# Kernel optimization log

Measured on AMD Instinct MI355X. Metric: run time of the kernel, lower is better.

The kernel has to match this reference:

```python
import jax, jax.numpy as jnp
import numpy as np

NUM_HEADS = 8


def setup_inputs() -> dict:
    key = jax.random.key(0)
    ks = jax.random.split(key, 6)
    B, S, H = 2, 4096, 512
    Q = jax.random.normal(ks[0], (B, S, H), dtype=jnp.float32)
    K = jax.random.normal(ks[1], (B, S, H), dtype=jnp.float32)
    V = jax.random.normal(ks[2], (B, S, H), dtype=jnp.float32)
    risk_sigma = jax.random.uniform(ks[3], (B, 1), dtype=jnp.float32) * 0.2
    risk_lambda = jnp.array([2.0], dtype=jnp.float32)
    W_out = jax.random.normal(ks[4], (H, H), dtype=jnp.float32) * (1.0 / np.sqrt(H))
    b_out = jnp.zeros((H,), dtype=jnp.float32)
    return {"Q": Q, "K": K, "V": V, "risk_sigma": risk_sigma,
            "risk_lambda": risk_lambda, "W_out": W_out, "b_out": b_out}


def reference(Q, K, V, risk_sigma, risk_lambda, W_out, b_out):
    B, S, H = Q.shape
    nh = NUM_HEADS
    hd = H // nh
    # split heads: [B, S, nh, hd]
    q = Q.reshape(B, S, nh, hd)
    k = K.reshape(B, S, nh, hd)
    v = V.reshape(B, S, nh, hd)
    scale = 1.0 / jnp.sqrt(jnp.asarray(hd, dtype=Q.dtype))
    # [B, nh, S, S]
    scores = jnp.einsum('bshd,bthd->bhst', q, k) * scale
    # distance-based risk penalty
    pos = jnp.arange(S, dtype=Q.dtype)
    norm_dist = jnp.abs(pos[None, :] - pos[:, None]) / S  # [S, S]
    dist_sq = norm_dist ** 2
    sigma_c = jnp.clip(risk_sigma, 0.001, 0.2)            # [B, 1]
    sigma_n = (sigma_c - 0.001) / (0.2 - 0.001)
    lam = (risk_lambda / 10.0).reshape(())                 # scalar
    risk_term = lam * sigma_n[:, :, None, None] * dist_sq[None, None]  # [B,1,S,S]
    attn = jax.nn.softmax(scores - risk_term, axis=-1)
    ctx = jnp.einsum('bhst,bthd->bshd', attn, v).reshape(B, S, H)
    return ctx @ W_out.T + b_out
```

## Files before the change

kernel.cpp:

```cpp
#include <hip/hip_runtime.h>
#include <hip/hip_bf16.h>


#define S_LEN 4096
#define NHEAD 8
#define HD 64
#define HTOT 512

typedef __attribute__((ext_vector_type(8))) short short8;
typedef __attribute__((ext_vector_type(4))) float floatx4;
typedef __attribute__((ext_vector_type(8))) _Float16 half8;
typedef __attribute__((ext_vector_type(2))) _Float16 half2v;

#if __has_builtin(__builtin_amdgcn_exp2f)
#define EXP2F(x) __builtin_amdgcn_exp2f(x)
#else
#define EXP2F(x) exp2f(x)
#endif

__device__ __forceinline__ unsigned pack_bf16(float a, float b) {
    unsigned ua = __builtin_bit_cast(unsigned, a) + 0x8000u;
    unsigned ub = __builtin_bit_cast(unsigned, b) + 0x8000u;
    return __builtin_amdgcn_perm(ub, ua, 0x07060302u);
}

__device__ __forceinline__ unsigned short f2bf(float x) {
    unsigned u = __builtin_bit_cast(unsigned, x) + 0x8000u;
    return (unsigned short)(u >> 16);
}

__device__ __forceinline__ void async16(const unsigned short* g, unsigned short* l) {
    __builtin_amdgcn_global_load_lds(
        (const __attribute__((address_space(1))) unsigned int*)g,
        (__attribute__((address_space(3))) unsigned int*)l, 16, 0, 0);
}

__global__ __launch_bounds__(256) void prep_kernel(
    const float* __restrict__ K, unsigned short* __restrict__ K16,
    const float* __restrict__ V, unsigned short* __restrict__ Vt,
    const float* __restrict__ W, unsigned short* __restrict__ W16)
{
    const int tid = threadIdx.x;
    if (blockIdx.x >= 3072) {
        size_t i = ((size_t)(blockIdx.x - 3072) * 256 + tid) * 8;
        float4 a = *(const float4*)(W + i);
        float4 b = *(const float4*)(W + i + 4);
        unsigned o[4] = {pack_bf16(a.x, a.y), pack_bf16(a.z, a.w),
                         pack_bf16(b.x, b.y), pack_bf16(b.z, b.w)};
        *(short8*)(W16 + i) = *(short8*)o;
    } else if (blockIdx.x < 2048) {
        size_t i = ((size_t)blockIdx.x * 256 + tid) * 8;
        float4 a = *(const float4*)(K + i);
        float4 b = *(const float4*)(K + i + 4);
        unsigned o[4] = {pack_bf16(a.x, a.y), pack_bf16(a.z, a.w),
                         pack_bf16(b.x, b.y), pack_bf16(b.z, b.w)};
        *(short8*)(K16 + i) = *(short8*)o;
    } else {
        __shared__ unsigned short T[64 * 66];
        const int blk = blockIdx.x - 2048;
        const int st = blk & 63;
        const int bh = blk >> 6;
        const int b = bh >> 3, h = bh & 7;
        const float* src = V + ((size_t)b * S_LEN + st * 64) * HTOT + h * HD;
        for (int i = 0; i < 4; i++) {
            int idx = tid + i * 256;
            int s = idx >> 4, c4 = idx & 15;
            float4 v = *(const float4*)(src + (size_t)s * HTOT + c4 * 4);
            T[(c4 * 4 + 0) * 66 + s] = f2bf(v.x);
            T[(c4 * 4 + 1) * 66 + s] = f2bf(v.y);
            T[(c4 * 4 + 2) * 66 + s] = f2bf(v.z);
            T[(c4 * 4 + 3) * 66 + s] = f2bf(v.w);
        }
        __syncthreads();
        unsigned short* dst = Vt + ((size_t)bh * 64) * S_LEN + st * 64;
        for (int i = 0; i < 2; i++) {
            int idx = tid + i * 256;
            int d = idx >> 3, c8 = idx & 7;
            uint2 lo = *(const uint2*)&T[d * 66 + c8 * 8];
            uint2 hi = *(const uint2*)&T[d * 66 + c8 * 8 + 4];
            unsigned o[4] = {lo.x, lo.y, hi.x, hi.y};
            *(short8*)(dst + (size_t)d * S_LEN + c8 * 8) = *(short8*)o;
        }
    }
}

__global__ __launch_bounds__(256) void attn_kernel(
    const float* __restrict__ Q, const unsigned short* __restrict__ K16,
    const unsigned short* __restrict__ Vt,
    const float* __restrict__ risk_sigma, const float* __restrict__ risk_lambda,
    _Float16* __restrict__ Cpart, float* __restrict__ Lpart)
{
    __shared__ unsigned short QPsh[128 * 72];
    __shared__ unsigned short Ksh[2][64 * 64];
    __shared__ unsigned short Vsh[2][64 * 64];

    const int tid  = threadIdx.x;
    const int wave = tid >> 6;
    const int lane = tid & 63;
    const int quad = lane >> 4;
    const int ln   = lane & 15;
    const int sw   = ln & 7;

    const int bid = blockIdx.x;
    const int ks  = bid & 1;
    const int qt  = (bid >> 1) & 31;
    const int h   = (bid >> 6) & 7;
    const int b   = bid >> 9;
    const int qbase = qt * 128;

    float sig = risk_sigma[b];
    sig = fminf(fmaxf(sig, 0.001f), 0.2f);
    const float sn   = (sig - 0.001f) * (1.0f / 0.199f);
    const float coef = risk_lambda[0] * 0.1f * sn;
    const float nc2 = -coef * (1.0f / 4096.0f) * (1.0f / 4096.0f) * 1.4426950408889634f;
    const float qscale = 0.125f * 1.4426950408889634f;

    const float* Qb = Q + (size_t)b * S_LEN * HTOT + (size_t)h * HD;
    const unsigned short* Kb = K16 + (size_t)b * S_LEN * HTOT + (size_t)h * HD;
    const unsigned short* Vb = Vt + ((size_t)(b * 8 + h) * 64) * S_LEN;

    const int rl  = lane >> 3;
    const int c8g = ((lane & 7) ^ rl) << 3;
    auto dma = [&](int buf, int kbase) {
        const unsigned short* gk = Kb + (size_t)(kbase + wave * 8 + rl) * HTOT + c8g;
        const unsigned short* gv = Vb + (size_t)(wave * 8 + rl) * S_LEN + kbase + c8g;
        async16(gk,              &Ksh[buf][wave * 512 + lane * 8]);
        async16(gk + 32 * HTOT,  &Ksh[buf][(wave + 4) * 512 + lane * 8]);
        async16(gv,              &Vsh[buf][wave * 512 + lane * 8]);
        async16(gv + 32 * S_LEN, &Vsh[buf][(wave + 4) * 512 + lane * 8]);
    };

    dma(0, ks * 2048);
    for (int i = 0; i < 8; i++) {
        int idx = tid + i * 256;
        int r = idx >> 4, c4 = idx & 15;
        float4 v = *(const float4*)(Qb + (size_t)(qbase + r) * HTOT + c4 * 4);
        uint2 o;
        o.x = pack_bf16(v.x * qscale, v.y * qscale);
        o.y = pack_bf16(v.z * qscale, v.w * qscale);
        *(uint2*)&QPsh[r * 72 + c4 * 4] = o;
    }
    __syncthreads();

    short8 qf[2][2];
    for (int nt = 0; nt < 2; nt++) {
        qf[nt][0] = *(const short8*)&QPsh[(wave * 32 + nt * 16 + ln) * 72 + quad * 8];
        qf[nt][1] = *(const short8*)&QPsh[(wave * 32 + nt * 16 + ln) * 72 + 32 + quad * 8];
    }
    unsigned short* Pw = &QPsh[wave * 32 * 72];

    const short sone = (short)0x3F80;
    const short8 ones = {sone, sone, sone, sone, sone, sone, sone, sone};

    floatx4 Oacc[2][4], Lacc[2];
    for (int nt = 0; nt < 2; nt++) {
        Lacc[nt] = (floatx4){0.f, 0.f, 0.f, 0.f};
        for (int dt = 0; dt < 4; dt++) Oacc[nt][dt] = (floatx4){0.f, 0.f, 0.f, 0.f};
    }

    const int qa = qbase + wave * 32;

    for (int kt = 0; kt < 32; ++kt) {
        const int kbase = ks * 2048 + kt * 64;
        const int cur = kt & 1;
        if (kt < 31) dma(1 - cur, kbase + 64);
        const unsigned short* Kc = Ksh[cur];
        const unsigned short* Vc = Vsh[cur];

        const float dq = (float)(qa + ln - kbase);
        for (int jt = 0; jt < 4; jt++) {
            const int krow = (jt * 16 + ln) * 64;
            short8 ak0 = *(const short8*)&Kc[krow + ((quad ^ sw) << 3)];
            short8 ak1 = *(const short8*)&Kc[krow + (((quad + 4) ^ sw) << 3)];
            #pragma unroll
            for (int nt = 0; nt < 2; nt++) {
                floatx4 s = (floatx4){0.f, 0.f, 0.f, 0.f};
                s = __builtin_amdgcn_mfma_f32_16x16x32_bf16(ak0, qf[nt][0], s, 0, 0, 0);
                s = __builtin_amdgcn_mfma_f32_16x16x32_bf16(ak1, qf[nt][1], s, 0, 0, 0);
                float d = dq + (float)(nt * 16 - jt * 16 - quad * 4);
                float p[4];
                #pragma unroll
                for (int r = 0; r < 4; r++) {
                    float arg = __builtin_fmaf(nc2, d * d, s[r]);
                    p[r] = EXP2F(arg);
                    d -= 1.0f;
                }
                uint2 o;
                o.x = pack_bf16(p[0], p[1]);
                o.y = pack_bf16(p[2], p[3]);
                *(uint2*)&Pw[(nt * 16 + ln) * 72 + jt * 16 + quad * 4] = o;
            }
        }
        asm volatile("s_waitcnt lgkmcnt(0)" ::: "memory");
        __builtin_amdgcn_wave_barrier();

        short8 pf[2][2];
        for (int nt = 0; nt < 2; nt++) {
            pf[nt][0] = *(const short8*)&Pw[(nt * 16 + ln) * 72 + quad * 8];
            pf[nt][1] = *(const short8*)&Pw[(nt * 16 + ln) * 72 + 32 + quad * 8];
        }
        for (int dt = 0; dt < 4; dt++) {
            const int vrow = (dt * 16 + ln) * 64;
            short8 bv0 = *(const short8*)&Vc[vrow + ((quad ^ sw) << 3)];
            short8 bv1 = *(const short8*)&Vc[vrow + (((quad + 4) ^ sw) << 3)];
            #pragma unroll
            for (int nt = 0; nt < 2; nt++) {
                Oacc[nt][dt] = __builtin_amdgcn_mfma_f32_16x16x32_bf16(pf[nt][0], bv0, Oacc[nt][dt], 0, 0, 0);
                Oacc[nt][dt] = __builtin_amdgcn_mfma_f32_16x16x32_bf16(pf[nt][1], bv1, Oacc[nt][dt], 0, 0, 0);
            }
        }
        #pragma unroll
        for (int nt = 0; nt < 2; nt++) {
            Lacc[nt] = __builtin_amdgcn_mfma_f32_16x16x32_bf16(pf[nt][0], ones, Lacc[nt], 0, 0, 0);
            Lacc[nt] = __builtin_amdgcn_mfma_f32_16x16x32_bf16(pf[nt][1], ones, Lacc[nt], 0, 0, 0);
        }
        __syncthreads();
    }

    _Float16* Cw = Cpart + (size_t)bid * (128 * 64);
    for (int nt = 0; nt < 2; nt++) {
        if (ln == 0) {
            #pragma unroll
            for (int r = 0; r < 4; r++)
                Lpart[bid * 128 + wave * 32 + nt * 16 + quad * 4 + r] = Lacc[nt][r];
        }
        float rl4[4];
        #pragma unroll
        for (int r = 0; r < 4; r++) rl4[r] = 1.0f / Lacc[nt][r];
        for (int dt = 0; dt < 4; dt++)
            #pragma unroll
            for (int r = 0; r < 4; r++) {
                int q = wave * 32 + nt * 16 + quad * 4 + r;
                Cw[q * 64 + dt * 16 + ln] = (_Float16)(Oacc[nt][dt][r] * rl4[r]);
            }
    }
}

__global__ __launch_bounds__(256) void combine_kernel(
    const _Float16* __restrict__ Cpart, const float* __restrict__ Lpart,
    unsigned short* __restrict__ ctx)
{
    const int t = threadIdx.x;
    const int tile = blockIdx.x;
    const int qt = tile & 31, h = (tile >> 5) & 7, b = tile >> 8;
    __shared__ float w0s[128], w1s[128];
    if (t < 128) {
        float l0 = Lpart[(tile * 2 + 0) * 128 + t];
        float l1 = Lpart[(tile * 2 + 1) * 128 + t];
        float inv = 1.0f / (l0 + l1);
        w0s[t] = l0 * inv;
        w1s[t] = l1 * inv;
    }
    __syncthreads();
    const _Float16* C0 = Cpart + (size_t)(tile * 2) * (128 * 64);
    const _Float16* C1 = C0 + 128 * 64;
    for (int i = 0; i < 8; i++) {
        int e = (i * 256 + t) * 4;
        int q = e >> 6, d = e & 63;
        half2v a0 = *(const half2v*)(C0 + e);
        half2v a1 = *(const half2v*)(C0 + e + 2);
        half2v b0 = *(const half2v*)(C1 + e);
        half2v b1 = *(const half2v*)(C1 + e + 2);
        float w0 = w0s[q], w1 = w1s[q];
        float v0 = w0 * (float)a0[0] + w1 * (float)b0[0];
        float v1 = w0 * (float)a0[1] + w1 * (float)b0[1];
        float v2 = w0 * (float)a1[0] + w1 * (float)b1[0];
        float v3 = w0 * (float)a1[1] + w1 * (float)b1[1];
        uint2 o;
        o.x = pack_bf16(v0, v1);
        o.y = pack_bf16(v2, v3);
        *(uint2*)&ctx[((size_t)b * S_LEN + qt * 128 + q) * HTOT + h * HD + d] = o;
    }
}

__global__ __launch_bounds__(256) void proj_kernel(
    const unsigned short* __restrict__ A,
    const unsigned short* __restrict__ W16,
    const float* __restrict__ bias,
    float* __restrict__ out)
{
    __shared__ unsigned short Ash[2][64 * 32];
    __shared__ unsigned short Bsh[2][128 * 32];
    const int tid = threadIdx.x;
    const int wave = tid >> 6, lane = tid & 63, quad = lane >> 4, ln = lane & 15;
    const int wr = wave >> 1, wc = wave & 1;
    const int m0 = blockIdx.y * 64;
    const int nb = blockIdx.x * 128;

    const int arow = (wave * 64 + lane) >> 2;
    const int ac   = (wave * 64 + lane) & 3;
    const int acs  = (ac ^ ((arow >> 1) & 3)) << 3;
    const int wrow0 = (wave * 64 + lane) >> 2;
    const int wc0   = (wave * 64 + lane) & 3;
    const int wcs0  = (wc0 ^ ((wrow0 >> 1) & 3)) << 3;
    const int wrow1 = wrow0 + 64;
    const int wcs1  = (wc0 ^ ((wrow1 >> 1) & 3)) << 3;

    auto dma = [&](int buf, int k0) {
        async16(A + (size_t)(m0 + arow) * 512 + k0 + acs,
                &Ash[buf][wave * 512 + lane * 8]);
        async16(W16 + (size_t)(nb + wrow0) * 512 + k0 + wcs0,
                &Bsh[buf][wave * 512 + lane * 8]);
        async16(W16 + (size_t)(nb + wrow1) * 512 + k0 + wcs1,
                &Bsh[buf][(wave + 4) * 512 + lane * 8]);
    };

    floatx4 acc[2][4];
    for (int i = 0; i < 2; i++)
        for (int j = 0; j < 4; j++) acc[i][j] = (floatx4){0.f, 0.f, 0.f, 0.f};

    dma(0, 0);
    for (int kt = 0; kt < 16; ++kt) {
        const int cur = kt & 1;
        __syncthreads();
        if (kt < 15) dma(1 - cur, (kt + 1) * 32);

        short8 af[2], bf[4];
        for (int i = 0; i < 2; i++) {
            int r = wr * 32 + i * 16 + ln;
            af[i] = *(const short8*)&Ash[cur][r * 32 + ((quad ^ ((r >> 1) & 3)) << 3)];
        }
        for (int j = 0; j < 4; j++) {
            int r = wc * 64 + j * 16 + ln;
            bf[j] = *(const short8*)&Bsh[cur][r * 32 + ((quad ^ ((r >> 1) & 3)) << 3)];
        }
        for (int i = 0; i < 2; i++)
            for (int j = 0; j < 4; j++)
                acc[i][j] = __builtin_amdgcn_mfma_f32_16x16x32_bf16(af[i], bf[j], acc[i][j], 0, 0, 0);
    }

    for (int i = 0; i < 2; i++) {
        int row = m0 + wr * 32 + i * 16 + quad * 4;
        for (int j = 0; j < 4; j++) {
            int col = nb + wc * 64 + j * 16 + ln;
            float bv = bias[col];
            #pragma unroll
            for (int r = 0; r < 4; r++)
                out[(size_t)(row + r) * 512 + col] = acc[i][j][r] + bv;
        }
    }
}

extern "C" void kernel_launch(void* const* d_in, const int* in_sizes, int n_in,
                              void* d_out, int out_size, void* d_ws, size_t ws_size,
                              hipStream_t stream) {
    const float* Q    = (const float*)d_in[0];
    const float* K    = (const float*)d_in[1];
    const float* V    = (const float*)d_in[2];
    const float* sig  = (const float*)d_in[3];
    const float* lam  = (const float*)d_in[4];
    const float* W    = (const float*)d_in[5];
    const float* bias = (const float*)d_in[6];

    unsigned short* K16 = (unsigned short*)d_ws;
    unsigned short* Vt  = (unsigned short*)((char*)d_ws + (8u << 20));
    unsigned short* ctx = (unsigned short*)((char*)d_ws + (16u << 20));
    float* Lpart        = (float*)((char*)d_ws + (24u << 20));
    unsigned short* W16 = (unsigned short*)((char*)d_ws + (24u << 20) + (512u << 10));
    _Float16* Cpart     = (_Float16*)d_out;
    float* out = (float*)d_out;

    prep_kernel<<<dim3(3200), dim3(256), 0, stream>>>(K, K16, V, Vt, W, W16);
    attn_kernel<<<dim3(1024), dim3(256), 0, stream>>>(Q, K16, Vt, sig, lam, Cpart, Lpart);
    combine_kernel<<<dim3(512), dim3(256), 0, stream>>>(Cpart, Lpart, ctx);
    proj_kernel<<<dim3(4, 128), dim3(256), 0, stream>>>(ctx, W16, bias, out);
}
```

Before: 228.9 us.

## Fuse split-K combine into projection GEMM and read V directly from global

Removes the separate combine kernel. The attention kernel now writes unnormalized fp16 partial outputs in [B,S,H] layout, and the projection kernel sums the two key-split partials, normalizes them with the summed L, and feeds fp16 MFMA with an fp16 W. V is no longer staged through LDS with async copies; each lane loads its V fragments straight from global memory, and occupancy is hinted with launch_bounds(256,4). V is pre-scaled by 0.25 to keep the fp16 partials in range. The changes trade one launch and one ctx round-trip for extra global traffic on V, plus fp16 range and precision risk.

```diff
diff --git a/kernel.cpp b/kernel.cpp
--- a/kernel.cpp
+++ b/kernel.cpp
@@ -10,7 +10,6 @@
 typedef __attribute__((ext_vector_type(8))) short short8;
 typedef __attribute__((ext_vector_type(4))) float floatx4;
 typedef __attribute__((ext_vector_type(8))) _Float16 half8;
-typedef __attribute__((ext_vector_type(2))) _Float16 half2v;
 
 #if __has_builtin(__builtin_amdgcn_exp2f)
 #define EXP2F(x) __builtin_amdgcn_exp2f(x)
@@ -38,16 +37,16 @@
 __global__ __launch_bounds__(256) void prep_kernel(
     const float* __restrict__ K, unsigned short* __restrict__ K16,
     const float* __restrict__ V, unsigned short* __restrict__ Vt,
-    const float* __restrict__ W, unsigned short* __restrict__ W16)
+    const float* __restrict__ W, _Float16* __restrict__ W16h)
 {
     const int tid = threadIdx.x;
     if (blockIdx.x >= 3072) {
         size_t i = ((size_t)(blockIdx.x - 3072) * 256 + tid) * 8;
         float4 a = *(const float4*)(W + i);
         float4 b = *(const float4*)(W + i + 4);
-        unsigned o[4] = {pack_bf16(a.x, a.y), pack_bf16(a.z, a.w),
-                         pack_bf16(b.x, b.y), pack_bf16(b.z, b.w)};
-        *(short8*)(W16 + i) = *(short8*)o;
+        half8 o = {(_Float16)a.x, (_Float16)a.y, (_Float16)a.z, (_Float16)a.w,
+                   (_Float16)b.x, (_Float16)b.y, (_Float16)b.z, (_Float16)b.w};
+        *(half8*)(W16h + i) = o;
     } else if (blockIdx.x < 2048) {
         size_t i = ((size_t)blockIdx.x * 256 + tid) * 8;
         float4 a = *(const float4*)(K + i);
@@ -66,10 +65,10 @@
             int idx = tid + i * 256;
             int s = idx >> 4, c4 = idx & 15;
             float4 v = *(const float4*)(src + (size_t)s * HTOT + c4 * 4);
-            T[(c4 * 4 + 0) * 66 + s] = f2bf(v.x);
-            T[(c4 * 4 + 1) * 66 + s] = f2bf(v.y);
-            T[(c4 * 4 + 2) * 66 + s] = f2bf(v.z);
-            T[(c4 * 4 + 3) * 66 + s] = f2bf(v.w);
+            T[(c4 * 4 + 0) * 66 + s] = f2bf(v.x * 0.25f);
+            T[(c4 * 4 + 1) * 66 + s] = f2bf(v.y * 0.25f);
+            T[(c4 * 4 + 2) * 66 + s] = f2bf(v.z * 0.25f);
+            T[(c4 * 4 + 3) * 66 + s] = f2bf(v.w * 0.25f);
         }
         __syncthreads();
         unsigned short* dst = Vt + ((size_t)bh * 64) * S_LEN + st * 64;
@@ -84,15 +83,14 @@
     }
 }
 
-__global__ __launch_bounds__(256) void attn_kernel(
+__global__ __launch_bounds__(256, 4) void attn_kernel(
     const float* __restrict__ Q, const unsigned short* __restrict__ K16,
     const unsigned short* __restrict__ Vt,
     const float* __restrict__ risk_sigma, const float* __restrict__ risk_lambda,
-    _Float16* __restrict__ Cpart, float* __restrict__ Lpart)
+    _Float16* __restrict__ Opart, float* __restrict__ Lpart)
 {
     __shared__ unsigned short QPsh[128 * 72];
     __shared__ unsigned short Ksh[2][64 * 64];
-    __shared__ unsigned short Vsh[2][64 * 64];
 
     const int tid  = threadIdx.x;
     const int wave = tid >> 6;
@@ -121,16 +119,13 @@
 
     const int rl  = lane >> 3;
     const int c8g = ((lane & 7) ^ rl) << 3;
-    auto dma = [&](int buf, int kbase) {
+    auto dmaK = [&](int buf, int kbase) {
         const unsigned short* gk = Kb + (size_t)(kbase + wave * 8 + rl) * HTOT + c8g;
-        const unsigned short* gv = Vb + (size_t)(wave * 8 + rl) * S_LEN + kbase + c8g;
-        async16(gk,              &Ksh[buf][wave * 512 + lane * 8]);
-        async16(gk + 32 * HTOT,  &Ksh[buf][(wave + 4) * 512 + lane * 8]);
-        async16(gv,              &Vsh[buf][wave * 512 + lane * 8]);
-        async16(gv + 32 * S_LEN, &Vsh[buf][(wave + 4) * 512 + lane * 8]);
+        async16(gk,             &Ksh[buf][wave * 512 + lane * 8]);
+        async16(gk + 32 * HTOT, &Ksh[buf][(wave + 4) * 512 + lane * 8]);
     };
 
-    dma(0, ks * 2048);
+    dmaK(0, ks * 2048);
     for (int i = 0; i < 8; i++) {
         int idx = tid + i * 256;
         int r = idx >> 4, c4 = idx & 15;
@@ -159,13 +154,13 @@
     }
 
     const int qa = qbase + wave * 32;
+    const unsigned short* vrow = Vb + (size_t)ln * S_LEN + quad * 8;
 
     for (int kt = 0; kt < 32; ++kt) {
         const int kbase = ks * 2048 + kt * 64;
         const int cur = kt & 1;
-        if (kt < 31) dma(1 - cur, kbase + 64);
+        if (kt < 31) dmaK(1 - cur, kbase + 64);
         const unsigned short* Kc = Ksh[cur];
-        const unsigned short* Vc = Vsh[cur];
 
         const float dq = (float)(qa + ln - kbase);
         for (int jt = 0; jt < 4; jt++) {
@@ -194,19 +189,23 @@
         asm volatile("s_waitcnt lgkmcnt(0)" ::: "memory");
         __builtin_amdgcn_wave_barrier();
 
+        short8 bv[4][2];
+        #pragma unroll
+        for (int dt = 0; dt < 4; dt++) {
+            const unsigned short* vp = vrow + (size_t)dt * 16 * S_LEN + kbase;
+            bv[dt][0] = *(const short8*)vp;
+            bv[dt][1] = *(const short8*)(vp + 32);
+        }
         short8 pf[2][2];
         for (int nt = 0; nt < 2; nt++) {
             pf[nt][0] = *(const short8*)&Pw[(nt * 16 + ln) * 72 + quad * 8];
             pf[nt][1] = *(const short8*)&Pw[(nt * 16 + ln) * 72 + 32 + quad * 8];
         }
         for (int dt = 0; dt < 4; dt++) {
-            const int vrow = (dt * 16 + ln) * 64;
-            short8 bv0 = *(const short8*)&Vc[vrow + ((quad ^ sw) << 3)];
-            short8 bv1 = *(const short8*)&Vc[vrow + (((quad + 4) ^ sw) << 3)];
             #pragma unroll
             for (int nt = 0; nt < 2; nt++) {
-                Oacc[nt][dt] = __builtin_amdgcn_mfma_f32_16x16x32_bf16(pf[nt][0], bv0, Oacc[nt][dt], 0, 0, 0);
-                Oacc[nt][dt] = __builtin_amdgcn_mfma_f32_16x16x32_bf16(pf[nt][1], bv1, Oacc[nt][dt], 0, 0, 0);
+                Oacc[nt][dt] = __builtin_amdgcn_mfma_f32_16x16x32_bf16(pf[nt][0], bv[dt][0], Oacc[nt][dt], 0, 0, 0);
+                Oacc[nt][dt] = __builtin_amdgcn_mfma_f32_16x16x32_bf16(pf[nt][1], bv[dt][1], Oacc[nt][dt], 0, 0, 0);
             }
         }
         #pragma unroll
@@ -217,116 +216,102 @@
         __syncthreads();
     }
 
-    _Float16* Cw = Cpart + (size_t)bid * (128 * 64);
+    _Float16* Ow = Opart + (size_t)ks * (S_LEN * 2 * HTOT);
+    float* Lw = Lpart + ks * 65536 + ((b * 8 + h) << 12);
     for (int nt = 0; nt < 2; nt++) {
         if (ln == 0) {
             #pragma unroll
             for (int r = 0; r < 4; r++)
-                Lpart[bid * 128 + wave * 32 + nt * 16 + quad * 4 + r] = Lacc[nt][r];
-        }
-        float rl4[4];
-        #pragma unroll
-        for (int r = 0; r < 4; r++) rl4[r] = 1.0f / Lacc[nt][r];
+                Lw[qa + nt * 16 + quad * 4 + r] = Lacc[nt][r];
+        }
         for (int dt = 0; dt < 4; dt++)
             #pragma unroll
             for (int r = 0; r < 4; r++) {
-                int q = wave * 32 + nt * 16 + quad * 4 + r;
-                Cw[q * 64 + dt * 16 + ln] = (_Float16)(Oacc[nt][dt][r] * rl4[r]);
+                int q = qa + nt * 16 + quad * 4 + r;
+                Ow[((size_t)b * S_LEN + q) * HTOT + h * HD + dt * 16 + ln] =
+                    (_Float16)Oacc[nt][dt][r];
             }
     }
 }
 
-__global__ __launch_bounds__(256) void combine_kernel(
-    const _Float16* __restrict__ Cpart, const float* __restrict__ Lpart,
-    unsigned short* __restrict__ ctx)
-{
-    const int t = threadIdx.x;
-    const int tile = blockIdx.x;
-    const int qt = tile & 31, h = (tile >> 5) & 7, b = tile >> 8;
-    __shared__ float w0s[128], w1s[128];
-    if (t < 128) {
-        float l0 = Lpart[(tile * 2 + 0) * 128 + t];
-        float l1 = Lpart[(tile * 2 + 1) * 128 + t];
-        float inv = 1.0f / (l0 + l1);
-        w0s[t] = l0 * inv;
-        w1s[t] = l1 * inv;
-    }
-    __syncthreads();
-    const _Float16* C0 = Cpart + (size_t)(tile * 2) * (128 * 64);
-    const _Float16* C1 = C0 + 128 * 64;
-    for (int i = 0; i < 8; i++) {
-        int e = (i * 256 + t) * 4;
-        int q = e >> 6, d = e & 63;
-        half2v a0 = *(const half2v*)(C0 + e);
-        half2v a1 = *(const half2v*)(C0 + e + 2);
-        half2v b0 = *(const half2v*)(C1 + e);
-        half2v b1 = *(const half2v*)(C1 + e + 2);
-        float w0 = w0s[q], w1 = w1s[q];
-        float v0 = w0 * (float)a0[0] + w1 * (float)b0[0];
-        float v1 = w0 * (float)a0[1] + w1 * (float)b0[1];
-        float v2 = w0 * (float)a1[0] + w1 * (float)b1[0];
-        float v3 = w0 * (float)a1[1] + w1 * (float)b1[1];
-        uint2 o;
-        o.x = pack_bf16(v0, v1);
-        o.y = pack_bf16(v2, v3);
-        *(uint2*)&ctx[((size_t)b * S_LEN + qt * 128 + q) * HTOT + h * HD + d] = o;
-    }
-}
-
 __global__ __launch_bounds__(256) void proj_kernel(
-    const unsigned short* __restrict__ A,
-    const unsigned short* __restrict__ W16,
-    const float* __restrict__ bias,
+    const _Float16* __restrict__ Opart, const float* __restrict__ Lpart,
+    const _Float16* __restrict__ W16h, const float* __restrict__ bias,
     float* __restrict__ out)
 {
     __shared__ unsigned short Ash[2][64 * 32];
     __shared__ unsigned short Bsh[2][128 * 32];
+    __shared__ float Lw[8][64];
+
     const int tid = threadIdx.x;
     const int wave = tid >> 6, lane = tid & 63, quad = lane >> 4, ln = lane & 15;
     const int wr = wave >> 1, wc = wave & 1;
     const int m0 = blockIdx.y * 64;
     const int nb = blockIdx.x * 128;
 
-    const int arow = (wave * 64 + lane) >> 2;
-    const int ac   = (wave * 64 + lane) & 3;
-    const int acs  = (ac ^ ((arow >> 1) & 3)) << 3;
+    for (int i = 0; i < 2; i++) {
+        int e = tid + i * 256;
+        int hh = e >> 6, r = e & 63;
+        int m = m0 + r, bb = m >> 12, q = m & 4095;
+        float l0 = Lpart[((bb * 8 + hh) << 12) + q];
+        float l1 = Lpart[65536 + ((bb * 8 + hh) << 12) + q];
+        Lw[hh][r] = 4.0f / (l0 + l1);
+    }
+
+    const _Float16* Op0 = Opart;
+    const _Float16* Op1 = Opart + (size_t)S_LEN * 2 * HTOT;
+
     const int wrow0 = (wave * 64 + lane) >> 2;
     const int wc0   = (wave * 64 + lane) & 3;
     const int wcs0  = (wc0 ^ ((wrow0 >> 1) & 3)) << 3;
     const int wrow1 = wrow0 + 64;
     const int wcs1  = (wc0 ^ ((wrow1 >> 1) & 3)) << 3;
-
-    auto dma = [&](int buf, int k0) {
-        async16(A + (size_t)(m0 + arow) * 512 + k0 + acs,
-                &Ash[buf][wave * 512 + lane * 8]);
-        async16(W16 + (size_t)(nb + wrow0) * 512 + k0 + wcs0,
+    auto dmaW = [&](int buf, int k0) {
+        async16((const unsigned short*)W16h + (size_t)(nb + wrow0) * 512 + k0 + wcs0,
                 &Bsh[buf][wave * 512 + lane * 8]);
-        async16(W16 + (size_t)(nb + wrow1) * 512 + k0 + wcs1,
+        async16((const unsigned short*)W16h + (size_t)(nb + wrow1) * 512 + k0 + wcs1,
                 &Bsh[buf][(wave + 4) * 512 + lane * 8]);
+    };
+
+    const int ar  = tid >> 2, ac8 = tid & 3;
+    const int asw = (ac8 ^ ((ar >> 1) & 3)) << 3;
+    auto stageA = [&](int buf, int k0) {
+        const int hh = k0 >> 6;
+        size_t off = (size_t)(m0 + ar) * 512 + k0 + ac8 * 8;
+        half8 o0 = *(const half8*)(Op0 + off);
+        half8 o1 = *(const half8*)(Op1 + off);
+        _Float16 lh = (_Float16)Lw[hh][ar];
+        half8 s = (o0 + o1) * lh;
+        *(half8*)&Ash[buf][ar * 32 + asw] = s;
     };
 
     floatx4 acc[2][4];
     for (int i = 0; i < 2; i++)
         for (int j = 0; j < 4; j++) acc[i][j] = (floatx4){0.f, 0.f, 0.f, 0.f};
 
-    dma(0, 0);
+    __syncthreads();
+    dmaW(0, 0);
+    stageA(0, 0);
+
     for (int kt = 0; kt < 16; ++kt) {
         const int cur = kt & 1;
         __syncthreads();
-        if (kt < 15) dma(1 - cur, (kt + 1) * 32);
-
-        short8 af[2], bf[4];
+        if (kt < 15) { dmaW(1 - cur, (kt + 1) * 32); stageA(1 - cur, (kt + 1) * 32); }
+
+        half8 af[2], bf[4];
         for (int i = 0; i < 2; i++) {
             int r = wr * 32 + i * 16 + ln;
-            af[i] = *(const short8*)&Ash[cur][r * 32 + ((quad ^ ((r >> 1) & 3)) << 3)];
+            af[i] = __builtin_bit_cast(half8,
+                *(const short8*)&Ash[cur][r * 32 + ((quad ^ ((r >> 1) & 3)) << 3)]);
         }
         for (int j = 0; j < 4; j++) {
             int r = wc * 64 + j * 16 + ln;
-            bf[j] = *(const short8*)&Bsh[cur][r * 32 + ((quad ^ ((r >> 1) & 3)) << 3)];
+            bf[j] = __builtin_bit_cast(half8,
+                *(const short8*)&Bsh[cur][r * 32 + ((quad ^ ((r >> 1) & 3)) << 3)]);
         }
         for (int i = 0; i < 2; i++)
             for (int j = 0; j < 4; j++)
-                acc[i][j] = __builtin_amdgcn_mfma_f32_16x16x32_bf16(af[i], bf[j], acc[i][j], 0, 0, 0);
+                acc[i][j] = __builtin_amdgcn_mfma_f32_16x16x32_f16(af[i], bf[j], acc[i][j], 0, 0, 0);
     }
 
     for (int i = 0; i < 2; i++) {
@@ -354,14 +339,12 @@
 
     unsigned short* K16 = (unsigned short*)d_ws;
     unsigned short* Vt  = (unsigned short*)((char*)d_ws + (8u << 20));
-    unsigned short* ctx = (unsigned short*)((char*)d_ws + (16u << 20));
-    float* Lpart        = (float*)((char*)d_ws + (24u << 20));
-    unsigned short* W16 = (unsigned short*)((char*)d_ws + (24u << 20) + (512u << 10));
-    _Float16* Cpart     = (_Float16*)d_out;
+    _Float16* Opart     = (_Float16*)((char*)d_ws + (16u << 20));
+    float* Lpart        = (float*)((char*)d_ws + (32u << 20));
+    _Float16* W16h      = (_Float16*)((char*)d_ws + (32u << 20) + (512u << 10));
     float* out = (float*)d_out;
 
-    prep_kernel<<<dim3(3200), dim3(256), 0, stream>>>(K, K16, V, Vt, W, W16);
-    attn_kernel<<<dim3(1024), dim3(256), 0, stream>>>(Q, K16, Vt, sig, lam, Cpart, Lpart);
-    combine_kernel<<<dim3(512), dim3(256), 0, stream>>>(Cpart, Lpart, ctx);
-    proj_kernel<<<dim3(4, 128), dim3(256), 0, stream>>>(ctx, W16, bias, out);
-}
+    prep_kernel<<<dim3(3200), dim3(256), 0, stream>>>(K, K16, V, Vt, W, W16h);
+    attn_kernel<<<dim3(1024), dim3(256), 0, stream>>>(Q, K16, Vt, sig, lam, Opart, Lpart);
+    proj_kernel<<<dim3(4, 128), dim3(256), 0, stream>>>(Opart, Lpart, W16h, bias, out);
+}
```

Measured after the change: 247.7 us. +8.2%, slower.
